# Kernel optimization log

Measured on AMD Instinct MI355X. Metric: run time of the kernel, lower is better.

Reference implementation:

```python
import math
import jax, jax.numpy as jnp
import numpy as np

TOP_K = 2
NUM_EXPERTS = 64
D_MODEL = 2048
CAP_FACTOR_EVAL = 2.0  # expert_capacity[1], eval mode (training=False)
ALPHA = 0.01
AUX_LOSS_WEIGHT = 1.0
Z_LOSS_WEIGHT = 1.0


def setup_inputs() -> dict:
    key = jax.random.key(0)
    k1, k2 = jax.random.split(key)
    inputs = jax.random.normal(k1, (4, 4096, D_MODEL), dtype=jnp.float32)
    # gate: nn.Linear(d_model, num_experts)
    W = jax.random.normal(k2, (NUM_EXPERTS, D_MODEL), dtype=jnp.float32) * (1.0 / math.sqrt(D_MODEL))
    b = jnp.zeros((NUM_EXPERTS,), dtype=jnp.float32)
    return {"inputs": inputs, "W": W, "b": b}


def reference(inputs, W, b):
    orig_dtype = inputs.dtype
    B, S, D = inputs.shape
    total_tokens = B * S
    x = inputs.astype(jnp.float32).reshape(total_tokens, D)
    # gate linear -> [T, E]
    router_logits = x @ W.T + b
    router_prob = jax.nn.softmax(router_logits, axis=-1)
    # top-k expert selection per token
    _, topk_idxs = jax.lax.top_k(router_prob, TOP_K)  # [T, top_k]
    rows = jnp.arange(total_tokens)[:, None]
    topk_expert_mask = jnp.zeros_like(router_prob).at[rows, topk_idxs].set(1.0)
    # auxiliary load-balancing loss (Switch Transformer)
    aux_loss = ALPHA * NUM_EXPERTS * jnp.dot(topk_expert_mask.mean(axis=0), router_prob.mean(axis=0))
    # z-loss (ST-MoE)
    z_loss = jnp.mean(jax.nn.logsumexp(router_logits, axis=-1) ** 2)
    loss = AUX_LOSS_WEIGHT * aux_loss + Z_LOSS_WEIGHT * z_loss
    # capacity limiting via cumulative position within each expert
    position_in_expert = jnp.cumsum(topk_expert_mask, axis=0) * topk_expert_mask
    expert_capacity = math.ceil(total_tokens / NUM_EXPERTS * CAP_FACTOR_EVAL)
    capped_mask = topk_expert_mask * (position_in_expert < expert_capacity)
    topk_weight = (router_prob * capped_mask).astype(orig_dtype)
    return capped_mask, topk_weight, loss
```

## Files before the change

kernel.cpp:

```cpp
#include <hip/hip_runtime.h>

#define TT 16384
#define DD 2048
#define EE 64
#define KSPLIT 4
#define KSL (DD/KSPLIT)
#define TM 64
#define NBLK (TT/TM)
#define CAP 512u

typedef __attribute__((ext_vector_type(8))) short bf16x8;
typedef __attribute__((ext_vector_type(4))) float f32x4;

__device__ __forceinline__ unsigned short f2bf(float x) {
    unsigned u = __float_as_uint(x);
    unsigned r = (u + 0x7fffu + ((u >> 16) & 1u)) >> 16;
    return (unsigned short)r;
}
__device__ __forceinline__ float bf2f(unsigned short b) {
    return __uint_as_float(((unsigned)b) << 16);
}

__device__ __forceinline__ bool pair_gt(float va, int ia, float vb, int ib) {
    return (va > vb) || (va == vb && ia < ib);
}

__device__ __forceinline__ void gload_lds16(const void* g, void* l) {
    __builtin_amdgcn_global_load_lds(
        (const __attribute__((address_space(1))) void*)g,
        (__attribute__((address_space(3))) void*)l,
        16, 0, 0);
}

__global__ __launch_bounds__(256) void k0_prep(
    const float* __restrict__ W, unsigned short* __restrict__ Wf)
{
    const int c = blockIdx.x * 256 + threadIdx.x;
    const int l = c & 63;
    const int t = (c >> 6) & 3;
    const int s = c >> 8;
    const int e = t * 16 + (l & 15);
    const int kk = s * 32 + (l >> 4) * 8;
    const float* wp = W + (size_t)e * DD + kk;
    unsigned short h[8], m[8], lo[8];
    #pragma unroll
    for (int j = 0; j < 8; ++j) {
        const float x = wp[j];
        h[j] = f2bf(x);
        const float r1 = x - bf2f(h[j]);
        m[j] = f2bf(r1);
        lo[j] = f2bf(r1 - bf2f(m[j]));
    }
    const size_t base = ((size_t)(s * 4 + t) * 3) * 64 + l;
    unsigned short* d0 = Wf + (base)      * 8;
    unsigned short* d1 = Wf + (base + 64) * 8;
    unsigned short* d2 = Wf + (base + 128) * 8;
    #pragma unroll
    for (int j = 0; j < 8; ++j) { d0[j] = h[j]; d1[j] = m[j]; d2[j] = lo[j]; }
}

__global__ __launch_bounds__(256, 6) void k1a_mfma(
    const float* __restrict__ X, const unsigned short* __restrict__ Wf,
    float* __restrict__ partial)
{
    __shared__ unsigned short Bs[2][12 * 512];

    const int tid = threadIdx.x;
    const int tb = blockIdx.x >> 2;
    const int sp = blockIdx.x & 3;
    const int wv = tid >> 6;
    const int l = tid & 63;
    const int tokb = tb * TM + wv * 16;
    const int row = tokb + (l & 15);

    const float* xp = X + (size_t)row * DD + sp * KSL + (l >> 4) * 8;
    const char* wfb = (const char*)Wf;
    const int c0 = wv * 3;
    const int sg0 = sp * 16;

    f32x4 acc[4];
    #pragma unroll
    for (int t = 0; t < 4; ++t) acc[t] = (f32x4){0.f, 0.f, 0.f, 0.f};

    #pragma unroll
    for (int c = 0; c < 3; ++c)
        gload_lds16(wfb + ((size_t)((sg0 + 0) * 12 + c0 + c) << 10) + (l << 4),
                    (char*)&Bs[0][0] + ((c0 + c) << 10));

    float4 xa = *(const float4*)(xp);
    float4 xb = *(const float4*)(xp + 4);
    __syncthreads();

    for (int s = 0; s < 16; ++s) {
        if (s + 1 < 16) {
            const int nb = (s + 1) & 1;
            #pragma unroll
            for (int c = 0; c < 3; ++c)
                gload_lds16(wfb + ((size_t)((sg0 + s + 1) * 12 + c0 + c) << 10) + (l << 4),
                            (char*)&Bs[nb][0] + ((c0 + c) << 10));
        }
        const int sn = (s + 1) & 15;
        const float4 na = *(const float4*)(xp + sn * 32);
        const float4 nb_ = *(const float4*)(xp + sn * 32 + 4);

        unsigned u[8] = {__float_as_uint(xa.x), __float_as_uint(xa.y),
                         __float_as_uint(xa.z), __float_as_uint(xa.w),
                         __float_as_uint(xb.x), __float_as_uint(xb.y),
                         __float_as_uint(xb.z), __float_as_uint(xb.w)};
        unsigned r1u[8], lfu[8];
        #pragma unroll
        for (int j = 0; j < 8; ++j) {
            const float xf = __uint_as_float(u[j]);
            const float hf = __uint_as_float(u[j] & 0xffff0000u);
            const float r1 = xf - hf;
            r1u[j] = __float_as_uint(r1);
            const float mf = __uint_as_float(r1u[j] & 0xffff0000u);
            lfu[j] = __float_as_uint(r1 - mf);
        }
        unsigned ah[4], am[4], al[4];
        #pragma unroll
        for (int d = 0; d < 4; ++d) {
            ah[d] = (u[2*d]   >> 16) | (u[2*d+1]   & 0xffff0000u);
            am[d] = (r1u[2*d] >> 16) | (r1u[2*d+1] & 0xffff0000u);
            al[d] = (lfu[2*d] >> 16) | (lfu[2*d+1] & 0xffff0000u);
        }
        typedef __attribute__((ext_vector_type(4))) unsigned uint4v;
        const bf16x8 Ah = __builtin_bit_cast(bf16x8, (uint4v){ah[0],ah[1],ah[2],ah[3]});
        const bf16x8 Am = __builtin_bit_cast(bf16x8, (uint4v){am[0],am[1],am[2],am[3]});
        const bf16x8 Al = __builtin_bit_cast(bf16x8, (uint4v){al[0],al[1],al[2],al[3]});

        const unsigned short* bb = &Bs[s & 1][l * 8];
        #pragma unroll
        for (int t = 0; t < 4; ++t) {
            bf16x8 B0 = *(const bf16x8*)(bb + (t * 3 + 0) * 512);
            bf16x8 B1 = *(const bf16x8*)(bb + (t * 3 + 1) * 512);
            bf16x8 B2 = *(const bf16x8*)(bb + (t * 3 + 2) * 512);
            acc[t] = __builtin_amdgcn_mfma_f32_16x16x32_bf16(Ah, B0, acc[t], 0, 0, 0);
            acc[t] = __builtin_amdgcn_mfma_f32_16x16x32_bf16(Ah, B1, acc[t], 0, 0, 0);
            acc[t] = __builtin_amdgcn_mfma_f32_16x16x32_bf16(Am, B0, acc[t], 0, 0, 0);
            acc[t] = __builtin_amdgcn_mfma_f32_16x16x32_bf16(Ah, B2, acc[t], 0, 0, 0);
            acc[t] = __builtin_amdgcn_mfma_f32_16x16x32_bf16(Am, B1, acc[t], 0, 0, 0);
            acc[t] = __builtin_amdgcn_mfma_f32_16x16x32_bf16(Al, B0, acc[t], 0, 0, 0);
        }
        __syncthreads();
        xa = na; xb = nb_;
    }

    #pragma unroll
    for (int t = 0; t < 4; ++t) {
        #pragma unroll
        for (int j = 0; j < 4; ++j) {
            const int tok = tokb + (l >> 4) * 4 + j;
            partial[((size_t)sp * TT + tok) * EE + t * 16 + (l & 15)] = acc[t][j];
        }
    }
}

__global__ __launch_bounds__(512) void k1b_epilogue(
    const float* __restrict__ partial, const float* __restrict__ bias,
    uint4* __restrict__ top2, unsigned* __restrict__ counts,
    float* __restrict__ probsum, float* __restrict__ zsum)
{
    __shared__ float Es[TM][EE + 1];
    __shared__ float lseS[TM];
    __shared__ unsigned cnt[EE];

    const int tid = threadIdx.x;
    const int b = blockIdx.x;
    const int tok0 = b * TM;
    const int tok = tid >> 3;
    const int o = tid & 7;
    const int e0 = o * 8;

    if (tid < EE) cnt[tid] = 0;
    __syncthreads();

    float f[8] = {0.f,0.f,0.f,0.f,0.f,0.f,0.f,0.f};
    #pragma unroll
    for (int sp = 0; sp < KSPLIT; ++sp) {
        const float* p = partial + ((size_t)sp * TT + tok0 + tok) * EE + e0;
        const float4 a = *(const float4*)(p);
        const float4 c = *(const float4*)(p + 4);
        f[0]+=a.x; f[1]+=a.y; f[2]+=a.z; f[3]+=a.w;
        f[4]+=c.x; f[5]+=c.y; f[6]+=c.z; f[7]+=c.w;
    }
    #pragma unroll
    for (int j = 0; j < 8; ++j) f[j] += bias[e0 + j];

    float mx = f[0];
    #pragma unroll
    for (int j = 1; j < 8; ++j) mx = fmaxf(mx, f[j]);
    #pragma unroll
    for (int sft = 1; sft < 8; sft <<= 1) mx = fmaxf(mx, __shfl_xor(mx, sft, 64));
    float sum = 0.f;
    #pragma unroll
    for (int j = 0; j < 8; ++j) sum += expf(f[j] - mx);
    #pragma unroll
    for (int sft = 1; sft < 8; sft <<= 1) sum += __shfl_xor(sum, sft, 64);
    const float lse = mx + logf(sum);

    float v1 = f[0]; int i1 = e0;
    float v2 = -3.402823466e38f; int i2 = 0x7fffffff;
    #pragma unroll
    for (int j = 1; j < 8; ++j) {
        const float vv = f[j]; const int e = e0 + j;
        if (pair_gt(vv, e, v1, i1)) { v2 = v1; i2 = i1; v1 = vv; i1 = e; }
        else if (pair_gt(vv, e, v2, i2)) { v2 = vv; i2 = e; }
    }
    #pragma unroll
    for (int sft = 1; sft < 8; sft <<= 1) {
        const float ov1 = __shfl_xor(v1, sft, 64); const int oi1 = __shfl_xor(i1, sft, 64);
        const float ov2 = __shfl_xor(v2, sft, 64); const int oi2 = __shfl_xor(i2, sft, 64);
        if (pair_gt(ov1, oi1, v1, i1)) {
            if (pair_gt(v1, i1, ov2, oi2)) { v2 = v1; i2 = i1; }
            else                            { v2 = ov2; i2 = oi2; }
            v1 = ov1; i1 = oi1;
        } else {
            if (pair_gt(ov1, oi1, v2, i2)) { v2 = ov1; i2 = oi1; }
        }
    }

    #pragma unroll
    for (int j = 0; j < 8; ++j) Es[tok][e0 + j] = expf(f[j] - lse);

    if (o == 0) {
        lseS[tok] = lse;
        top2[tok0 + tok] = make_uint4((unsigned)i1, (unsigned)i2,
                                      __float_as_uint(expf(v1 - lse)),
                                      __float_as_uint(expf(v2 - lse)));
        atomicAdd(&cnt[i1], 1u);
        atomicAdd(&cnt[i2], 1u);
    }
    __syncthreads();

    if (tid < EE) {
        float s = 0.f;
        for (int t = 0; t < TM; ++t) s += Es[t][tid];
        probsum[b * EE + tid] = s;
        counts[b * EE + tid] = cnt[tid];
    }
    if (tid >= 64 && tid < 128) {
        const int t = tid - 64;
        float z = lseS[t]; z = z * z;
        #pragma unroll
        for (int sft = 1; sft < 64; sft <<= 1) z += __shfl_xor(z, sft, 64);
        if (t == 0) zsum[b] = z;
    }
}

__global__ __launch_bounds__(256) void k2_scan(
    const unsigned* __restrict__ counts, const float* __restrict__ probsum,
    const float* __restrict__ zsum, unsigned* __restrict__ base,
    float* __restrict__ loss_out)
{
    __shared__ unsigned pc[4][EE];
    __shared__ float pps[4][EE];
    __shared__ float zz[256];
    const int tid = threadIdx.x;
    const int e = tid & 63, q = tid >> 6;
    const int b0 = q * (NBLK / 4), b1 = b0 + (NBLK / 4);

    unsigned csum = 0; float psum_ = 0.f;
    for (int bb = b0; bb < b1; ++bb) {
        csum += counts[bb * EE + e];
        psum_ += probsum[bb * EE + e];
    }
    pc[q][e] = csum; pps[q][e] = psum_;
    zz[tid] = zsum[tid];
    __syncthreads();

    unsigned off = 0;
    for (int qq = 0; qq < q; ++qq) off += pc[qq][e];
    unsigned run = off;
    for (int bb = b0; bb < b1; ++bb) {
        base[bb * EE + e] = run;
        run += counts[bb * EE + e];
    }

    if (q == 0) {
        const unsigned tot = pc[0][e] + pc[1][e] + pc[2][e] + pc[3][e];
        const float pt = pps[0][e] + pps[1][e] + pps[2][e] + pps[3][e];
        float a = (float)tot * pt;
        #pragma unroll
        for (int sft = 1; sft < 64; sft <<= 1) a += __shfl_xor(a, sft, 64);
        float z4 = zz[tid] + zz[tid + 64] + zz[tid + 128] + zz[tid + 192];
        #pragma unroll
        for (int sft = 1; sft < 64; sft <<= 1) z4 += __shfl_xor(z4, sft, 64);
        if (e == 0) {
            const float Tf = (float)TT;
            loss_out[0] = 0.01f * 64.0f * (a / (Tf * Tf)) + z4 / Tf;
        }
    }
}

__global__ __launch_bounds__(256) void k3_write(
    const uint4* __restrict__ top2, const unsigned* __restrict__ base,
    float* __restrict__ mask_out, float* __restrict__ w_out)
{
    __shared__ unsigned ti1[TM], ti2[TM], tk1[TM], tk2[TM];
    __shared__ float tw1[TM], tw2[TM];
    const int b = blockIdx.x, tid = threadIdx.x;
    if (tid < TM) {
        const uint4 v = top2[b * TM + tid];
        ti1[tid] = v.x; ti2[tid] = v.y;
        tw1[tid] = __uint_as_float(v.z); tw2[tid] = __uint_as_float(v.w);
    }
    __syncthreads();
    if (tid < EE) {
        const unsigned e = (unsigned)tid;
        unsigned cc = base[b * EE + tid];
        for (int i = 0; i < TM; ++i) {
            if (ti1[i] == e) { cc++; tk1[i] = (cc < CAP); }
            if (ti2[i] == e) { cc++; tk2[i] = (cc < CAP); }
        }
    }
    __syncthreads();
    const int i = tid >> 2, q = tid & 3;
    const unsigned a1 = ti1[i], a2 = ti2[i];
    const unsigned kp1 = tk1[i], kp2 = tk2[i];
    const float w1 = tw1[i], w2 = tw2[i];
    float om[16], ow[16];
    #pragma unroll
    for (int j = 0; j < 16; ++j) {
        const unsigned e = (unsigned)(q * 16 + j);
        float mv = 0.f, wv = 0.f;
        if (e == a1 && kp1) { mv = 1.f; wv = w1; }
        if (e == a2 && kp2) { mv = 1.f; wv = w2; }
        om[j] = mv; ow[j] = wv;
    }
    float* mrow = mask_out + (size_t)(b * TM + i) * EE + q * 16;
    float* wrow = w_out    + (size_t)(b * TM + i) * EE + q * 16;
    #pragma unroll
    for (int j4 = 0; j4 < 4; ++j4) {
        *(float4*)(mrow + j4 * 4) = make_float4(om[j4*4+0], om[j4*4+1], om[j4*4+2], om[j4*4+3]);
        *(float4*)(wrow + j4 * 4) = make_float4(ow[j4*4+0], ow[j4*4+1], ow[j4*4+2], ow[j4*4+3]);
    }
}

extern "C" void kernel_launch(void* const* d_in, const int* in_sizes, int n_in,
                              void* d_out, int out_size, void* d_ws, size_t ws_size,
                              hipStream_t stream)
{
    const float* X    = (const float*)d_in[0];
    const float* W    = (const float*)d_in[1];
    const float* bias = (const float*)d_in[2];
    float* out = (float*)d_out;
    float* mask_out = out;
    float* w_out    = out + (size_t)TT * EE;
    float* loss_out = out + (size_t)2 * TT * EE;

    char* ws = (char*)d_ws;
    unsigned short* Wf = (unsigned short*)ws;
    float*    partial = (float*)(ws + 1048576);
    size_t off = 1048576 + (size_t)KSPLIT * TT * EE * 4;
    uint4*    top2    = (uint4*)(ws + off);      off += (size_t)TT * 16;
    unsigned* counts  = (unsigned*)(ws + off);   off += (size_t)NBLK * EE * 4;
    float*    probsum = (float*)(ws + off);      off += (size_t)NBLK * EE * 4;
    float*    zsum    = (float*)(ws + off);      off += 4096;
    unsigned* base    = (unsigned*)(ws + off);

    k0_prep<<<64, 256, 0, stream>>>(W, Wf);
    k1a_mfma<<<NBLK * KSPLIT, 256, 0, stream>>>(X, Wf, partial);
    k1b_epilogue<<<NBLK, 512, 0, stream>>>(partial, bias, top2, counts, probsum, zsum);
    k2_scan<<<1, 256, 0, stream>>>(counts, probsum, zsum, base, loss_out);
    k3_write<<<NBLK, 256, 0, stream>>>(top2, base, mask_out, w_out);
}
```

Measured before the change: 62.02 us.

## Give each wave two 16-token row tiles to reuse B fragments

Each wave of the gate GEMM now computes two 16-row token tiles instead of one, and the block shrinks from four waves to two while keeping 64 tokens per block. Every weight fragment read from LDS now feeds two MFMA chains, which halves LDS reads per MFMA and interleaves independent accumulators to hide MFMA latency. Each wave also issues twice as many weight loads into LDS per stage. The cost is higher register pressure, with the occupancy hint changed to 3, and fewer waves per block to hide global loads of X.

```diff
diff --git a/kernel.cpp b/kernel.cpp
--- a/kernel.cpp
+++ b/kernel.cpp
@@ -5,12 +5,15 @@
 #define EE 64
 #define KSPLIT 4
 #define KSL (DD/KSPLIT)
+#define TMA 64
+#define NTB (TT/TMA)
 #define TM 64
 #define NBLK (TT/TM)
 #define CAP 512u
 
 typedef __attribute__((ext_vector_type(8))) short bf16x8;
 typedef __attribute__((ext_vector_type(4))) float f32x4;
+typedef __attribute__((ext_vector_type(4))) unsigned uint4v;
 
 __device__ __forceinline__ unsigned short f2bf(float x) {
     unsigned u = __float_as_uint(x);
@@ -30,6 +33,35 @@
         (const __attribute__((address_space(1))) void*)g,
         (__attribute__((address_space(3))) void*)l,
         16, 0, 0);
+}
+
+__device__ __forceinline__ void split3(const float4& a, const float4& b,
+                                       bf16x8& H, bf16x8& M, bf16x8& L)
+{
+    unsigned u[8] = {__float_as_uint(a.x), __float_as_uint(a.y),
+                     __float_as_uint(a.z), __float_as_uint(a.w),
+                     __float_as_uint(b.x), __float_as_uint(b.y),
+                     __float_as_uint(b.z), __float_as_uint(b.w)};
+    unsigned r1u[8], lfu[8];
+    #pragma unroll
+    for (int j = 0; j < 8; ++j) {
+        const float xf = __uint_as_float(u[j]);
+        const float hf = __uint_as_float(u[j] & 0xffff0000u);
+        const float r1 = xf - hf;
+        r1u[j] = __float_as_uint(r1);
+        const float mf = __uint_as_float(r1u[j] & 0xffff0000u);
+        lfu[j] = __float_as_uint(r1 - mf);
+    }
+    unsigned ah[4], am[4], al[4];
+    #pragma unroll
+    for (int d = 0; d < 4; ++d) {
+        ah[d] = (u[2*d]   >> 16) | (u[2*d+1]   & 0xffff0000u);
+        am[d] = (r1u[2*d] >> 16) | (r1u[2*d+1] & 0xffff0000u);
+        al[d] = (lfu[2*d] >> 16) | (lfu[2*d+1] & 0xffff0000u);
+    }
+    H = __builtin_bit_cast(bf16x8, (uint4v){ah[0], ah[1], ah[2], ah[3]});
+    M = __builtin_bit_cast(bf16x8, (uint4v){am[0], am[1], am[2], am[3]});
+    L = __builtin_bit_cast(bf16x8, (uint4v){al[0], al[1], al[2], al[3]});
 }
 
 __global__ __launch_bounds__(256) void k0_prep(
@@ -59,7 +91,7 @@
     for (int j = 0; j < 8; ++j) { d0[j] = h[j]; d1[j] = m[j]; d2[j] = lo[j]; }
 }
 
-__global__ __launch_bounds__(256, 6) void k1a_mfma(
+__global__ __launch_bounds__(128, 3) void k1a_mfma(
     const float* __restrict__ X, const unsigned short* __restrict__ Wf,
     float* __restrict__ partial)
 {
@@ -70,64 +102,49 @@
     const int sp = blockIdx.x & 3;
     const int wv = tid >> 6;
     const int l = tid & 63;
-    const int tokb = tb * TM + wv * 16;
-    const int row = tokb + (l & 15);
-
-    const float* xp = X + (size_t)row * DD + sp * KSL + (l >> 4) * 8;
+    const int tokb = tb * TMA + wv * 32;
+    const int row0 = tokb + (l & 15);
+
+    const float* xp0 = X + (size_t)row0 * DD + sp * KSL + (l >> 4) * 8;
+    const float* xp1 = xp0 + 16 * DD;
     const char* wfb = (const char*)Wf;
-    const int c0 = wv * 3;
     const int sg0 = sp * 16;
-
-    f32x4 acc[4];
-    #pragma unroll
-    for (int t = 0; t < 4; ++t) acc[t] = (f32x4){0.f, 0.f, 0.f, 0.f};
-
-    #pragma unroll
-    for (int c = 0; c < 3; ++c)
-        gload_lds16(wfb + ((size_t)((sg0 + 0) * 12 + c0 + c) << 10) + (l << 4),
+    const int c0 = wv * 6;
+
+    f32x4 acc0[4], acc1[4];
+    #pragma unroll
+    for (int t = 0; t < 4; ++t) {
+        acc0[t] = (f32x4){0.f, 0.f, 0.f, 0.f};
+        acc1[t] = (f32x4){0.f, 0.f, 0.f, 0.f};
+    }
+
+    #pragma unroll
+    for (int c = 0; c < 6; ++c)
+        gload_lds16(wfb + ((size_t)(sg0 * 12 + c0 + c) << 10) + (l << 4),
                     (char*)&Bs[0][0] + ((c0 + c) << 10));
-
-    float4 xa = *(const float4*)(xp);
-    float4 xb = *(const float4*)(xp + 4);
+    float4 xa0 = *(const float4*)(xp0);
+    float4 xb0 = *(const float4*)(xp0 + 4);
+    float4 xa1 = *(const float4*)(xp1);
+    float4 xb1 = *(const float4*)(xp1 + 4);
     __syncthreads();
 
     for (int s = 0; s < 16; ++s) {
         if (s + 1 < 16) {
             const int nb = (s + 1) & 1;
             #pragma unroll
-            for (int c = 0; c < 3; ++c)
+            for (int c = 0; c < 6; ++c)
                 gload_lds16(wfb + ((size_t)((sg0 + s + 1) * 12 + c0 + c) << 10) + (l << 4),
                             (char*)&Bs[nb][0] + ((c0 + c) << 10));
         }
         const int sn = (s + 1) & 15;
-        const float4 na = *(const float4*)(xp + sn * 32);
-        const float4 nb_ = *(const float4*)(xp + sn * 32 + 4);
-
-        unsigned u[8] = {__float_as_uint(xa.x), __float_as_uint(xa.y),
-                         __float_as_uint(xa.z), __float_as_uint(xa.w),
-                         __float_as_uint(xb.x), __float_as_uint(xb.y),
-                         __float_as_uint(xb.z), __float_as_uint(xb.w)};
-        unsigned r1u[8], lfu[8];
-        #pragma unroll
-        for (int j = 0; j < 8; ++j) {
-            const float xf = __uint_as_float(u[j]);
-            const float hf = __uint_as_float(u[j] & 0xffff0000u);
-            const float r1 = xf - hf;
-            r1u[j] = __float_as_uint(r1);
-            const float mf = __uint_as_float(r1u[j] & 0xffff0000u);
-            lfu[j] = __float_as_uint(r1 - mf);
-        }
-        unsigned ah[4], am[4], al[4];
-        #pragma unroll
-        for (int d = 0; d < 4; ++d) {
-            ah[d] = (u[2*d]   >> 16) | (u[2*d+1]   & 0xffff0000u);
-            am[d] = (r1u[2*d] >> 16) | (r1u[2*d+1] & 0xffff0000u);
-            al[d] = (lfu[2*d] >> 16) | (lfu[2*d+1] & 0xffff0000u);
-        }
-        typedef __attribute__((ext_vector_type(4))) unsigned uint4v;
-        const bf16x8 Ah = __builtin_bit_cast(bf16x8, (uint4v){ah[0],ah[1],ah[2],ah[3]});
-        const bf16x8 Am = __builtin_bit_cast(bf16x8, (uint4v){am[0],am[1],am[2],am[3]});
-        const bf16x8 Al = __builtin_bit_cast(bf16x8, (uint4v){al[0],al[1],al[2],al[3]});
+        const float4 na0 = *(const float4*)(xp0 + sn * 32);
+        const float4 nb0 = *(const float4*)(xp0 + sn * 32 + 4);
+        const float4 na1 = *(const float4*)(xp1 + sn * 32);
+        const float4 nb1 = *(const float4*)(xp1 + sn * 32 + 4);
+
+        bf16x8 Ah0, Am0, Al0, Ah1, Am1, Al1;
+        split3(xa0, xb0, Ah0, Am0, Al0);
+        split3(xa1, xb1, Ah1, Am1, Al1);
 
         const unsigned short* bb = &Bs[s & 1][l * 8];
         #pragma unroll
@@ -135,23 +152,30 @@
             bf16x8 B0 = *(const bf16x8*)(bb + (t * 3 + 0) * 512);
             bf16x8 B1 = *(const bf16x8*)(bb + (t * 3 + 1) * 512);
             bf16x8 B2 = *(const bf16x8*)(bb + (t * 3 + 2) * 512);
-            acc[t] = __builtin_amdgcn_mfma_f32_16x16x32_bf16(Ah, B0, acc[t], 0, 0, 0);
-            acc[t] = __builtin_amdgcn_mfma_f32_16x16x32_bf16(Ah, B1, acc[t], 0, 0, 0);
-            acc[t] = __builtin_amdgcn_mfma_f32_16x16x32_bf16(Am, B0, acc[t], 0, 0, 0);
-            acc[t] = __builtin_amdgcn_mfma_f32_16x16x32_bf16(Ah, B2, acc[t], 0, 0, 0);
-            acc[t] = __builtin_amdgcn_mfma_f32_16x16x32_bf16(Am, B1, acc[t], 0, 0, 0);
-            acc[t] = __builtin_amdgcn_mfma_f32_16x16x32_bf16(Al, B0, acc[t], 0, 0, 0);
+            acc0[t] = __builtin_amdgcn_mfma_f32_16x16x32_bf16(Ah0, B0, acc0[t], 0, 0, 0);
+            acc1[t] = __builtin_amdgcn_mfma_f32_16x16x32_bf16(Ah1, B0, acc1[t], 0, 0, 0);
+            acc0[t] = __builtin_amdgcn_mfma_f32_16x16x32_bf16(Ah0, B1, acc0[t], 0, 0, 0);
+            acc1[t] = __builtin_amdgcn_mfma_f32_16x16x32_bf16(Ah1, B1, acc1[t], 0, 0, 0);
+            acc0[t] = __builtin_amdgcn_mfma_f32_16x16x32_bf16(Am0, B0, acc0[t], 0, 0, 0);
+            acc1[t] = __builtin_amdgcn_mfma_f32_16x16x32_bf16(Am1, B0, acc1[t], 0, 0, 0);
+            acc0[t] = __builtin_amdgcn_mfma_f32_16x16x32_bf16(Ah0, B2, acc0[t], 0, 0, 0);
+            acc1[t] = __builtin_amdgcn_mfma_f32_16x16x32_bf16(Ah1, B2, acc1[t], 0, 0, 0);
+            acc0[t] = __builtin_amdgcn_mfma_f32_16x16x32_bf16(Am0, B1, acc0[t], 0, 0, 0);
+            acc1[t] = __builtin_amdgcn_mfma_f32_16x16x32_bf16(Am1, B1, acc1[t], 0, 0, 0);
+            acc0[t] = __builtin_amdgcn_mfma_f32_16x16x32_bf16(Al0, B0, acc0[t], 0, 0, 0);
+            acc1[t] = __builtin_amdgcn_mfma_f32_16x16x32_bf16(Al1, B0, acc1[t], 0, 0, 0);
         }
         __syncthreads();
-        xa = na; xb = nb_;
+        xa0 = na0; xb0 = nb0; xa1 = na1; xb1 = nb1;
     }
 
     #pragma unroll
     for (int t = 0; t < 4; ++t) {
         #pragma unroll
         for (int j = 0; j < 4; ++j) {
-            const int tok = tokb + (l >> 4) * 4 + j;
-            partial[((size_t)sp * TT + tok) * EE + t * 16 + (l & 15)] = acc[t][j];
+            const int tok0_ = tokb + (l >> 4) * 4 + j;
+            partial[((size_t)sp * TT + tok0_) * EE + t * 16 + (l & 15)] = acc0[t][j];
+            partial[((size_t)sp * TT + tok0_ + 16) * EE + t * 16 + (l & 15)] = acc1[t][j];
         }
     }
 }
@@ -360,7 +384,7 @@
     unsigned* base    = (unsigned*)(ws + off);
 
     k0_prep<<<64, 256, 0, stream>>>(W, Wf);
-    k1a_mfma<<<NBLK * KSPLIT, 256, 0, stream>>>(X, Wf, partial);
+    k1a_mfma<<<NTB * KSPLIT, 128, 0, stream>>>(X, Wf, partial);
     k1b_epilogue<<<NBLK, 512, 0, stream>>>(partial, bias, top2, counts, probsum, zsum);
     k2_scan<<<1, 256, 0, stream>>>(counts, probsum, zsum, base, loss_out);
     k3_write<<<NBLK, 256, 0, stream>>>(top2, base, mask_out, w_out);
```

Result: slower. 63.98 us (+3.2%).
